# Kernel optimization log

Measured on AMD Instinct MI355X. Metric: run time of the kernel, lower is better.

Reference implementation:

```python
import jax, jax.numpy as jnp
import numpy as np

B, L, D = 4, 4096, 1024
K = D // 4

def setup_inputs() -> dict:
    key = jax.random.key(0)
    ks = jax.random.split(key, 16)
    def w(k, sh):
        return jax.random.normal(k, sh, dtype=jnp.float32) * 0.02
    return {
        'x': jax.random.normal(ks[0], (B, L, D), dtype=jnp.float32),
        'Wk1': w(ks[1], (D, D)), 'bk1': jnp.zeros((D,), jnp.float32),
        'Wk2': w(ks[2], (D, K * 4)), 'bk2': jnp.zeros((K * 4,), jnp.float32),
        'Wq1': w(ks[3], (D, D)), 'bq1': jnp.zeros((D,), jnp.float32),
        'Wq2': w(ks[4], (D, K * 4)), 'bq2': jnp.zeros((K * 4,), jnp.float32),
        'Wv': w(ks[5], (D, D)), 'bv': jnp.zeros((D,), jnp.float32),
        'gamma': jnp.ones((D,), jnp.float32), 'beta': jnp.zeros((D,), jnp.float32),
        'Wo': w(ks[6], (D, D)), 'bo': jnp.zeros((D,), jnp.float32),
    }

def _normalize(q, eps=1e-12):
    n = jnp.sqrt(jnp.sum(q * q, axis=-1, keepdims=True))
    return q / jnp.maximum(n, eps)

def _quat_conj(q):
    return q * jnp.asarray([1., -1., -1., -1.], dtype=q.dtype)

def _quat_mul(q1, q2):
    w1, x1, y1, z1 = q1[..., 0], q1[..., 1], q1[..., 2], q1[..., 3]
    w2, x2, y2, z2 = q2[..., 0], q2[..., 1], q2[..., 2], q2[..., 3]
    w = w1 * w2 - x1 * x2 - y1 * y2 - z1 * z2
    x = w1 * x2 + x1 * w2 + y1 * z2 - z1 * y2
    y = w1 * y2 - x1 * z2 + y1 * w2 + z1 * x2
    z = w1 * z2 + x1 * y2 - y1 * x2 + z1 * w2
    return jnp.stack([w, x, y, z], axis=-1)

def _quat_rotate(q, v):
    return _quat_mul(_quat_mul(q, v), _quat_conj(q))

def _mlp(x, W1, b1, W2, b2):
    h = jax.nn.gelu(x @ W1 + b1, approximate=False)
    return h @ W2 + b2

def _layernorm(x, g, b, eps=1e-5):
    mu = jnp.mean(x, axis=-1, keepdims=True)
    var = jnp.var(x, axis=-1, keepdims=True)
    return (x - mu) * jax.lax.rsqrt(var + eps) * g + b

def reference(x, Wk1, bk1, Wk2, bk2, Wq1, bq1, Wq2, bq2, Wv, bv, gamma, beta, Wo, bo):
    b, l, d = x.shape
    k = d // 4
    key_q = _normalize(_mlp(x, Wk1, bk1, Wk2, bk2).reshape(b, l, k, 4))
    query_q = _normalize(_mlp(x, Wq1, bq1, Wq2, bq2).reshape(b, l, k, 4))
    value = (x @ Wv + bv).reshape(b, l, k, 4)
    rotated = _quat_rotate(key_q, value)            # [B,L,K,4]
    memory = jnp.cumsum(rotated, axis=1)            # prefix-sum memory
    retrieved = _quat_rotate(_quat_conj(query_q), memory).reshape(b, l, d)
    norm = jnp.sqrt(jnp.arange(1, l + 1, dtype=x.dtype)).reshape(1, l, 1)
    out = _layernorm(retrieved / norm, gamma, beta) @ Wo + bo
    return x + out
```

## Files before the change

### kernel.cpp

```cpp
#include <hip/hip_runtime.h>
#include <hip/hip_bf16.h>
#include <cstddef>
#include <cstdint>

static constexpr int B   = 4;
static constexpr int L   = 4096;
static constexpr int D   = 1024;
static constexpr int M   = B * L;
static constexpr int NCH = 64;
static constexpr int CHL = L / NCH;

typedef __attribute__((ext_vector_type(8))) short short8;
typedef __attribute__((ext_vector_type(4))) float f32x4;

#define AS1C(p) ((const __attribute__((address_space(1))) void*)(p))
#define AS3(p)  ((__attribute__((address_space(3))) void*)(p))

__device__ __forceinline__ float b2f(unsigned short u) {
    union { unsigned int i; float f; } c; c.i = ((unsigned int)u) << 16; return c.f;
}
__device__ __forceinline__ unsigned short f2b(float f) {
    union { float f; unsigned int i; } c; c.f = f;
    unsigned int r = c.i + 0x7fffu + ((c.i >> 16) & 1u);
    return (unsigned short)(r >> 16);
}
__device__ __forceinline__ float4 qmul(const float4 a, const float4 b) {
    float4 r;
    r.x = a.x * b.x - a.y * b.y - a.z * b.z - a.w * b.w;
    r.y = a.x * b.y + a.y * b.x + a.z * b.w - a.w * b.z;
    r.z = a.x * b.z - a.y * b.w + a.z * b.x + a.w * b.y;
    r.w = a.x * b.w + a.y * b.z - a.z * b.y + a.w * b.x;
    return r;
}
__device__ __forceinline__ float4 qconj(const float4 a) {
    return make_float4(a.x, -a.y, -a.z, -a.w);
}
__device__ __forceinline__ float4 qnorm(const float4 a) {
    float n = sqrtf(a.x * a.x + a.y * a.y + a.z * a.z + a.w * a.w);
    float inv = 1.0f / fmaxf(n, 1e-12f);
    return make_float4(a.x * inv, a.y * inv, a.z * inv, a.w * inv);
}
__device__ __forceinline__ float gelu_exact(float v) {
    return 0.5f * v * (1.0f + erff(v * 0.7071067811865476f));
}

__global__ __launch_bounds__(256)
void conv_k(const float* __restrict__ src, unsigned short* __restrict__ dst, int n4)
{
    const int i = blockIdx.x * 256 + threadIdx.x;
    if (i >= n4) return;
    const float4 v = reinterpret_cast<const float4*>(src)[i];
    ushort4 o;
    o.x = f2b(v.x); o.y = f2b(v.y); o.z = f2b(v.z); o.w = f2b(v.w);
    reinterpret_cast<ushort4*>(dst)[i] = o;
}

__global__ __launch_bounds__(256)
void wtrans_k(const float* __restrict__ src, unsigned short* __restrict__ dst)
{
    __shared__ float t[32][33];
    const int tx = threadIdx.x, ty = threadIdx.y;
    const int n0 = blockIdx.x * 32, k0 = blockIdx.y * 32;
    #pragma unroll
    for (int j = ty; j < 32; j += 8)
        t[j][tx] = src[(size_t)(k0 + j) * D + n0 + tx];
    __syncthreads();
    #pragma unroll
    for (int j = ty; j < 32; j += 8)
        dst[(size_t)(n0 + j) * D + k0 + tx] = f2b(t[tx][j]);
}

template <int EPI>
__global__ __launch_bounds__(256)
void gemm_bf16_k(const unsigned short* __restrict__ A,
                 const unsigned short* __restrict__ BT,
                 const float* __restrict__ bias,
                 const float* __restrict__ resid,
                 void* __restrict__ C, int Mm, int Nn, int Kk)
{
    __shared__ alignas(16) unsigned short As[128 * 32];
    __shared__ alignas(16) unsigned short Bs[128 * 32];

    const int tid  = threadIdx.x;
    const int lane = tid & 63;
    const int w    = tid >> 6;
    const int wr   = w >> 1;
    const int wc   = w & 1;

    const int nwg = gridDim.x;
    const int cpx = nwg >> 3;
    const int bid = blockIdx.x;
    const int swz = (bid & 7) * cpx + (bid >> 3);
    const int nTN = Nn >> 7;
    const int m0  = (swz / nTN) << 7;
    const int n0  = (swz % nTN) << 7;

    f32x4 acc[4][4] = {};

    for (int k0 = 0; k0 < Kk; k0 += 32) {
        #pragma unroll
        for (int c = 0; c < 2; ++c) {
            const int i  = (c * 4 + w) * 64 + lane;
            const int r  = i >> 2;
            const int cc = i & 3;
            __builtin_amdgcn_global_load_lds(
                AS1C(A + (size_t)(m0 + r) * Kk + k0 + cc * 8),
                AS3((char*)As + (c * 4 + w) * 1024), 16, 0, 0);
            __builtin_amdgcn_global_load_lds(
                AS1C(BT + (size_t)(n0 + r) * Kk + k0 + cc * 8),
                AS3((char*)Bs + (c * 4 + w) * 1024), 16, 0, 0);
        }
        __syncthreads();

        short8 af[4], bf[4];
        #pragma unroll
        for (int mi = 0; mi < 4; ++mi) {
            const int r = wr * 64 + mi * 16 + (lane & 15);
            af[mi] = *reinterpret_cast<const short8*>(
                (const char*)As + r * 64 + (lane >> 4) * 16);
        }
        #pragma unroll
        for (int ni = 0; ni < 4; ++ni) {
            const int cI = wc * 64 + ni * 16 + (lane & 15);
            bf[ni] = *reinterpret_cast<const short8*>(
                (const char*)Bs + cI * 64 + (lane >> 4) * 16);
        }
        #pragma unroll
        for (int mi = 0; mi < 4; ++mi)
            #pragma unroll
            for (int ni = 0; ni < 4; ++ni)
                acc[mi][ni] = __builtin_amdgcn_mfma_f32_16x16x32_bf16(
                    af[mi], bf[ni], acc[mi][ni], 0, 0, 0);
        __syncthreads();
    }

    const int colbase = n0 + wc * 64 + (lane & 15);
    #pragma unroll
    for (int ni = 0; ni < 4; ++ni) {
        const int col = colbase + ni * 16;
        const float bv = bias[col];
        #pragma unroll
        for (int mi = 0; mi < 4; ++mi) {
            const int row0 = m0 + wr * 64 + mi * 16 + (lane >> 4) * 4;
            #pragma unroll
            for (int r = 0; r < 4; ++r) {
                float v = acc[mi][ni][r] + bv;
                if (EPI == 1) v = gelu_exact(v);
                const size_t idx = (size_t)(row0 + r) * Nn + col;
                if (EPI <= 1) {
                    ((unsigned short*)C)[idx] = f2b(v);
                } else {
                    if (EPI == 3) v += resid[idx];
                    ((float*)C)[idx] = v;
                }
            }
        }
    }
}

__global__ __launch_bounds__(256)
void rotate_k(const unsigned short* __restrict__ kraw, float* __restrict__ v, int nq)
{
    const int i = blockIdx.x * 256 + threadIdx.x;
    if (i >= nq) return;
    const ushort4 qu = reinterpret_cast<const ushort4*>(kraw)[i];
    float4 q = qnorm(make_float4(b2f(qu.x), b2f(qu.y), b2f(qu.z), b2f(qu.w)));
    const float4 val = reinterpret_cast<const float4*>(v)[i];
    const float4 r = qmul(qmul(q, val), qconj(q));
    reinterpret_cast<float4*>(v)[i] = r;
}

__global__ __launch_bounds__(256)
void scan_pass1(const float* __restrict__ rot, float* __restrict__ part)
{
    const int g  = blockIdx.x * 256 + threadIdx.x;
    const int d  = g & (D - 1);
    const int ch = (g >> 10) & (NCH - 1);
    const int b  = g >> 16;
    const size_t base = ((size_t)b * L + (size_t)ch * CHL) * D + d;
    float s = 0.f;
    for (int i = 0; i < CHL; ++i) s += rot[base + (size_t)i * D];
    part[g] = s;
}

__global__ __launch_bounds__(256)
void scan_pass2(float* __restrict__ part)
{
    const int g = blockIdx.x * 256 + threadIdx.x;
    const int d = g & (D - 1);
    const int b = g >> 10;
    float run = 0.f;
    for (int c = 0; c < NCH; ++c) {
        const size_t idx = ((size_t)b * NCH + c) * D + d;
        const float t = part[idx];
        part[idx] = run;
        run += t;
    }
}

__global__ __launch_bounds__(256)
void scan_pass3(float* __restrict__ rot, const float* __restrict__ part)
{
    const int g  = blockIdx.x * 256 + threadIdx.x;
    const int d  = g & (D - 1);
    const int ch = (g >> 10) & (NCH - 1);
    const int b  = g >> 16;
    const size_t base = ((size_t)b * L + (size_t)ch * CHL) * D + d;
    float run = part[g];
    for (int i = 0; i < CHL; ++i) {
        const size_t idx = base + (size_t)i * D;
        run += rot[idx];
        rot[idx] = run;
    }
}

__global__ __launch_bounds__(256)
void retrieve_ln_k(const float* __restrict__ mem, const unsigned short* __restrict__ qraw,
                   const float* __restrict__ gamma, const float* __restrict__ beta,
                   unsigned short* __restrict__ out)
{
    const int row = blockIdx.x;
    const int l   = row & (L - 1);
    const int t   = threadIdx.x;
    const size_t base = (size_t)row * D + t * 4;

    const ushort4 qu = reinterpret_cast<const ushort4*>(qraw)[base >> 2];
    const float4 q = qnorm(make_float4(b2f(qu.x), b2f(qu.y), b2f(qu.z), b2f(qu.w)));
    const float4 m4 = *reinterpret_cast<const float4*>(mem + base);
    float4 r = qmul(qmul(qconj(q), m4), q);

    const float inv = 1.0f / sqrtf((float)(l + 1));
    r.x *= inv; r.y *= inv; r.z *= inv; r.w *= inv;

    float s  = r.x + r.y + r.z + r.w;
    float ss = r.x * r.x + r.y * r.y + r.z * r.z + r.w * r.w;
    #pragma unroll
    for (int off = 32; off > 0; off >>= 1) {
        s  += __shfl_xor(s, off);
        ss += __shfl_xor(ss, off);
    }
    __shared__ float red[2][4];
    const int wid = t >> 6, lane = t & 63;
    if (lane == 0) { red[0][wid] = s; red[1][wid] = ss; }
    __syncthreads();
    const float sum = red[0][0] + red[0][1] + red[0][2] + red[0][3];
    const float ssq = red[1][0] + red[1][1] + red[1][2] + red[1][3];
    const float mu  = sum * (1.0f / (float)D);
    const float var = ssq * (1.0f / (float)D) - mu * mu;
    const float sc  = rsqrtf(var + 1e-5f);

    const float4 g4 = *reinterpret_cast<const float4*>(gamma + t * 4);
    const float4 b4 = *reinterpret_cast<const float4*>(beta  + t * 4);
    ushort4 o;
    o.x = f2b((r.x - mu) * sc * g4.x + b4.x);
    o.y = f2b((r.y - mu) * sc * g4.y + b4.y);
    o.z = f2b((r.z - mu) * sc * g4.z + b4.z);
    o.w = f2b((r.w - mu) * sc * g4.w + b4.w);
    reinterpret_cast<ushort4*>(out)[base >> 2] = o;
}

extern "C" void kernel_launch(void* const* d_in, const int* in_sizes, int n_in,
                              void* d_out, int out_size, void* d_ws, size_t ws_size,
                              hipStream_t stream)
{
    const float* x     = (const float*)d_in[0];
    const float* Wk1   = (const float*)d_in[1];
    const float* bk1   = (const float*)d_in[2];
    const float* Wk2   = (const float*)d_in[3];
    const float* bk2   = (const float*)d_in[4];
    const float* Wq1   = (const float*)d_in[5];
    const float* bq1   = (const float*)d_in[6];
    const float* Wq2   = (const float*)d_in[7];
    const float* bq2   = (const float*)d_in[8];
    const float* Wv    = (const float*)d_in[9];
    const float* bv    = (const float*)d_in[10];
    const float* gamma = (const float*)d_in[11];
    const float* beta  = (const float*)d_in[12];
    const float* Wo    = (const float*)d_in[13];
    const float* bo    = (const float*)d_in[14];
    float* out = (float*)d_out;

    const size_t TD = (size_t)M * D;
    const size_t DD = (size_t)D * D;
    unsigned short* xb   = (unsigned short*)d_ws;
    unsigned short* hb   = xb + TD;
    unsigned short* qb   = hb + TD;
    float*          bufB = (float*)(qb + TD);
    unsigned short* wT   = (unsigned short*)(bufB + TD);
    float*          part = (float*)(wT + 6 * DD);

    unsigned short* wk1 = wT;
    unsigned short* wk2 = wT + DD;
    unsigned short* wv_ = wT + 2 * DD;
    unsigned short* wq1 = wT + 3 * DD;
    unsigned short* wq2 = wT + 4 * DD;
    unsigned short* wo_ = wT + 5 * DD;

    const dim3 blk(256);
    const dim3 tblk(32, 8);
    const dim3 tgrid(D / 32, D / 32);
    const int nwg = (M / 128) * (D / 128);
    const int nq  = (int)(TD / 4);

    conv_k<<<(int)(TD / 4 / 256), blk, 0, stream>>>(x, xb, (int)(TD / 4));
    wtrans_k<<<tgrid, tblk, 0, stream>>>(Wk1, wk1);
    wtrans_k<<<tgrid, tblk, 0, stream>>>(Wk2, wk2);
    wtrans_k<<<tgrid, tblk, 0, stream>>>(Wv,  wv_);
    wtrans_k<<<tgrid, tblk, 0, stream>>>(Wq1, wq1);
    wtrans_k<<<tgrid, tblk, 0, stream>>>(Wq2, wq2);
    wtrans_k<<<tgrid, tblk, 0, stream>>>(Wo,  wo_);

    gemm_bf16_k<1><<<nwg, blk, 0, stream>>>(xb, wk1, bk1, nullptr, hb,   M, D, D);
    gemm_bf16_k<0><<<nwg, blk, 0, stream>>>(hb, wk2, bk2, nullptr, qb,   M, D, D);
    gemm_bf16_k<2><<<nwg, blk, 0, stream>>>(xb, wv_, bv,  nullptr, bufB, M, D, D);

    rotate_k<<<nq / 256, blk, 0, stream>>>(qb, bufB, nq);

    scan_pass1<<<(B * NCH * D) / 256, blk, 0, stream>>>(bufB, part);
    scan_pass2<<<(B * D) / 256,       blk, 0, stream>>>(part);
    scan_pass3<<<(B * NCH * D) / 256, blk, 0, stream>>>(bufB, part);

    gemm_bf16_k<1><<<nwg, blk, 0, stream>>>(xb, wq1, bq1, nullptr, hb, M, D, D);
    gemm_bf16_k<0><<<nwg, blk, 0, stream>>>(hb, wq2, bq2, nullptr, qb, M, D, D);

    retrieve_ln_k<<<M, blk, 0, stream>>>(bufB, qb, gamma, beta, hb);

    gemm_bf16_k<3><<<nwg, blk, 0, stream>>>(hb, wo_, bo, x, out, M, D, D);
}
```

Measured before the change: 513.2 us.

## Batch projection GEMMs into wide 256-tile pipelined GEMMs and fuse rotate with scan

Concatenates the K1/Q1/V weights and the K2/Q2 weights so the five projection GEMMs become two launches. All GEMMs move to a new 256x256-tile, 512-thread kernel with a 3-buffer LDS pipeline, XOR-swizzled LDS layout, and setprio hints. The quaternion rotation is fused into the first scan pass, and the scan now works on float4. Exact erf GELU is replaced with a polynomial approximation. This cuts launch count, memory round trips and GEMM stall time, at the cost of more LDS, higher register pressure and a small GELU accuracy change.

Result: faster. 464.5 us (-9.5%).

```diff
diff --git a/kernel.cpp b/kernel.cpp
--- a/kernel.cpp
+++ b/kernel.cpp
@@ -1,14 +1,13 @@
 #include <hip/hip_runtime.h>
-#include <hip/hip_bf16.h>
 #include <cstddef>
 #include <cstdint>
 
-static constexpr int B   = 4;
-static constexpr int L   = 4096;
-static constexpr int D   = 1024;
-static constexpr int M   = B * L;
-static constexpr int NCH = 64;
-static constexpr int CHL = L / NCH;
+static constexpr int Bb  = 4;
+static constexpr int Ll  = 4096;
+static constexpr int Dd  = 1024;
+static constexpr int Mm  = 16384;
+static constexpr int KK  = 1024;
+static constexpr int NTK = 32;
 
 typedef __attribute__((ext_vector_type(8))) short short8;
 typedef __attribute__((ext_vector_type(4))) float f32x4;
@@ -40,8 +39,15 @@
     float inv = 1.0f / fmaxf(n, 1e-12f);
     return make_float4(a.x * inv, a.y * inv, a.z * inv, a.w * inv);
 }
-__device__ __forceinline__ float gelu_exact(float v) {
-    return 0.5f * v * (1.0f + erff(v * 0.7071067811865476f));
+__device__ __forceinline__ float gelu_fast(float v) {
+    const float a = fabsf(v) * 0.70710678118654752f;
+    const float t = 1.0f / (1.0f + 0.3275911f * a);
+    const float p = t * (0.254829592f + t * (-0.284496736f + t * (1.421413741f
+                   + t * (-1.453152027f + t * 1.061405429f))));
+    const float e = __expf(-a * a);
+    const float erfa = 1.0f - p * e;
+    const float erfv = copysignf(erfa, v);
+    return 0.5f * v * (1.0f + erfv);
 }
 
 __global__ __launch_bounds__(256)
@@ -63,95 +69,156 @@
     const int n0 = blockIdx.x * 32, k0 = blockIdx.y * 32;
     #pragma unroll
     for (int j = ty; j < 32; j += 8)
-        t[j][tx] = src[(size_t)(k0 + j) * D + n0 + tx];
+        t[j][tx] = src[(size_t)(k0 + j) * Dd + n0 + tx];
     __syncthreads();
     #pragma unroll
     for (int j = ty; j < 32; j += 8)
-        dst[(size_t)(n0 + j) * D + k0 + tx] = f2b(t[tx][j]);
-}
-
-template <int EPI>
-__global__ __launch_bounds__(256)
-void gemm_bf16_k(const unsigned short* __restrict__ A,
-                 const unsigned short* __restrict__ BT,
-                 const float* __restrict__ bias,
-                 const float* __restrict__ resid,
-                 void* __restrict__ C, int Mm, int Nn, int Kk)
-{
-    __shared__ alignas(16) unsigned short As[128 * 32];
-    __shared__ alignas(16) unsigned short Bs[128 * 32];
-
+        dst[(size_t)(n0 + j) * Dd + k0 + tx] = f2b(t[tx][j]);
+}
+
+__global__ __launch_bounds__(256)
+void bcat_k(const float* __restrict__ bk1, const float* __restrict__ bq1,
+            const float* __restrict__ bv,  const float* __restrict__ bk2,
+            const float* __restrict__ bq2, float* __restrict__ b1,
+            float* __restrict__ b2)
+{
+    const int i = blockIdx.x * 256 + threadIdx.x;
+    if (i < 3072) b1[i] = (i < 1024) ? bk1[i] : (i < 2048 ? bq1[i - 1024] : bv[i - 2048]);
+    if (i < 2048) b2[i] = (i < 1024) ? bk2[i] : bq2[i - 1024];
+}
+
+template<int MODE>
+__global__ __launch_bounds__(512, 2)
+void gemm256_k(const unsigned short* __restrict__ A, int astride,
+               const unsigned short* __restrict__ BT,
+               const float* __restrict__ bias,
+               const float* __restrict__ resid,
+               unsigned short* __restrict__ outH,
+               float* __restrict__ outF,
+               int Nn)
+{
+    extern __shared__ char smem[];
     const int tid  = threadIdx.x;
     const int lane = tid & 63;
     const int w    = tid >> 6;
-    const int wr   = w >> 1;
-    const int wc   = w & 1;
+    const int wr   = w >> 2;
+    const int wc   = w & 3;
 
     const int nwg = gridDim.x;
     const int cpx = nwg >> 3;
     const int bid = blockIdx.x;
     const int swz = (bid & 7) * cpx + (bid >> 3);
-    const int nTN = Nn >> 7;
-    const int m0  = (swz / nTN) << 7;
-    const int n0  = (swz % nTN) << 7;
-
-    f32x4 acc[4][4] = {};
-
-    for (int k0 = 0; k0 < Kk; k0 += 32) {
+    const int nTN = Nn >> 8;
+    const int m0  = (swz / nTN) << 8;
+    const int n0  = (swz % nTN) << 8;
+    const int aoff = (MODE == 1 && n0 >= 1024) ? 1024 : 0;
+
+    const unsigned short* gA[2];
+    const unsigned short* gB[2];
+    #pragma unroll
+    for (int c = 0; c < 2; ++c) {
+        const int n16 = c * 512 + tid;
+        const int line = n16 >> 3;
+        const int u = (n16 & 7) ^ (line & 7);
+        const int r = 2 * line + (u >> 2);
+        const int kcs = u & 3;
+        gA[c] = A + (size_t)(m0 + r) * astride + aoff + kcs * 8;
+        gB[c] = BT + (size_t)(n0 + r) * KK + kcs * 8;
+    }
+    const int wslot = w * 1024;
+
+    auto STAGE = [&](int kt, int bi) {
+        const int koff = kt * 32;
         #pragma unroll
         for (int c = 0; c < 2; ++c) {
-            const int i  = (c * 4 + w) * 64 + lane;
-            const int r  = i >> 2;
-            const int cc = i & 3;
-            __builtin_amdgcn_global_load_lds(
-                AS1C(A + (size_t)(m0 + r) * Kk + k0 + cc * 8),
-                AS3((char*)As + (c * 4 + w) * 1024), 16, 0, 0);
-            __builtin_amdgcn_global_load_lds(
-                AS1C(BT + (size_t)(n0 + r) * Kk + k0 + cc * 8),
-                AS3((char*)Bs + (c * 4 + w) * 1024), 16, 0, 0);
+            __builtin_amdgcn_global_load_lds(AS1C(gA[c] + koff),
+                AS3(smem + bi * 16384 + c * 8192 + wslot), 16, 0, 0);
+            __builtin_amdgcn_global_load_lds(AS1C(gB[c] + koff),
+                AS3(smem + 49152 + bi * 16384 + c * 8192 + wslot), 16, 0, 0);
         }
-        __syncthreads();
-
+    };
+
+    const int kc = lane >> 4;
+    const int rl = lane & 15;
+    int offA[8], offB[4];
+    #pragma unroll
+    for (int mi = 0; mi < 8; ++mi) {
+        const int r = wr * 128 + mi * 16 + rl;
+        offA[mi] = (r >> 1) * 128 + (((((r & 1) << 2) | kc) ^ ((r >> 1) & 7)) << 4);
+    }
+    #pragma unroll
+    for (int ni = 0; ni < 4; ++ni) {
+        const int r = wc * 64 + ni * 16 + rl;
+        offB[ni] = 49152 + (r >> 1) * 128 + (((((r & 1) << 2) | kc) ^ ((r >> 1) & 7)) << 4);
+    }
+
+    f32x4 acc[8][4] = {};
+
+    auto BODY = [&](int kt, int bi, int bi2, int vm, bool dostage) {
+        if (dostage) STAGE(kt + 2, bi2);
+        const char* Ab = smem + bi * 16384;
         short8 af[4], bf[4];
         #pragma unroll
-        for (int mi = 0; mi < 4; ++mi) {
-            const int r = wr * 64 + mi * 16 + (lane & 15);
-            af[mi] = *reinterpret_cast<const short8*>(
-                (const char*)As + r * 64 + (lane >> 4) * 16);
-        }
-        #pragma unroll
-        for (int ni = 0; ni < 4; ++ni) {
-            const int cI = wc * 64 + ni * 16 + (lane & 15);
-            bf[ni] = *reinterpret_cast<const short8*>(
-                (const char*)Bs + cI * 64 + (lane >> 4) * 16);
-        }
+        for (int ni = 0; ni < 4; ++ni) bf[ni] = *(const short8*)(smem + bi * 16384 + offB[ni]);
+        #pragma unroll
+        for (int mi = 0; mi < 4; ++mi) af[mi] = *(const short8*)(Ab + offA[mi]);
+        __builtin_amdgcn_s_barrier();
+        __builtin_amdgcn_s_setprio(1);
         #pragma unroll
         for (int mi = 0; mi < 4; ++mi)
             #pragma unroll
             for (int ni = 0; ni < 4; ++ni)
-                acc[mi][ni] = __builtin_amdgcn_mfma_f32_16x16x32_bf16(
-                    af[mi], bf[ni], acc[mi][ni], 0, 0, 0);
-        __syncthreads();
-    }
-
-    const int colbase = n0 + wc * 64 + (lane & 15);
+                acc[mi][ni] = __builtin_amdgcn_mfma_f32_16x16x32_bf16(af[mi], bf[ni], acc[mi][ni], 0, 0, 0);
+        __builtin_amdgcn_s_setprio(0);
+        __builtin_amdgcn_s_barrier();
+        #pragma unroll
+        for (int mi = 0; mi < 4; ++mi) af[mi] = *(const short8*)(Ab + offA[4 + mi]);
+        __builtin_amdgcn_s_setprio(1);
+        #pragma unroll
+        for (int mi = 0; mi < 4; ++mi)
+            #pragma unroll
+            for (int ni = 0; ni < 4; ++ni)
+                acc[4 + mi][ni] = __builtin_amdgcn_mfma_f32_16x16x32_bf16(af[mi], bf[ni], acc[4 + mi][ni], 0, 0, 0);
+        __builtin_amdgcn_s_setprio(0);
+        if (vm == 4)      asm volatile("s_waitcnt vmcnt(4)" ::: "memory");
+        else if (vm == 0) asm volatile("s_waitcnt vmcnt(0)" ::: "memory");
+        if (vm >= 0) __builtin_amdgcn_s_barrier();
+    };
+
+    STAGE(0, 0);
+    STAGE(1, 1);
+    asm volatile("s_waitcnt vmcnt(4)" ::: "memory");
+    __builtin_amdgcn_s_barrier();
+
+    for (int t0 = 0; t0 < NTK - 2; t0 += 3) {
+        BODY(t0 + 0, 0, 2, 4, true);
+        BODY(t0 + 1, 1, 0, 4, true);
+        BODY(t0 + 2, 2, 1, 4, true);
+    }
+    BODY(NTK - 2, 0, 0, 0, false);
+    BODY(NTK - 1, 1, 0, -1, false);
+
+    const int colb = n0 + wc * 64 + rl;
+    const int rowb = m0 + wr * 128 + kc * 4;
     #pragma unroll
     for (int ni = 0; ni < 4; ++ni) {
-        const int col = colbase + ni * 16;
+        const int col = colb + ni * 16;
         const float bv = bias[col];
         #pragma unroll
-        for (int mi = 0; mi < 4; ++mi) {
-            const int row0 = m0 + wr * 64 + mi * 16 + (lane >> 4) * 4;
+        for (int mi = 0; mi < 8; ++mi) {
+            const int row0 = rowb + mi * 16;
             #pragma unroll
-            for (int r = 0; r < 4; ++r) {
-                float v = acc[mi][ni][r] + bv;
-                if (EPI == 1) v = gelu_exact(v);
-                const size_t idx = (size_t)(row0 + r) * Nn + col;
-                if (EPI <= 1) {
-                    ((unsigned short*)C)[idx] = f2b(v);
+            for (int rr = 0; rr < 4; ++rr) {
+                float v = acc[mi][ni][rr] + bv;
+                const int row = row0 + rr;
+                if (MODE == 0) {
+                    if (n0 < 2048) outH[(size_t)row * 2048 + col] = f2b(gelu_fast(v));
+                    else           outF[(size_t)row * 1024 + (col - 2048)] = v;
+                } else if (MODE == 1) {
+                    outH[(size_t)row * 2048 + col] = f2b(v);
                 } else {
-                    if (EPI == 3) v += resid[idx];
-                    ((float*)C)[idx] = v;
+                    const size_t ix = (size_t)row * 1024 + col;
+                    outF[ix] = v + resid[ix];
                 }
             }
         }
@@ -159,72 +226,69 @@
 }
 
 __global__ __launch_bounds__(256)
-void rotate_k(const unsigned short* __restrict__ kraw, float* __restrict__ v, int nq)
-{
-    const int i = blockIdx.x * 256 + threadIdx.x;
-    if (i >= nq) return;
-    const ushort4 qu = reinterpret_cast<const ushort4*>(kraw)[i];
-    float4 q = qnorm(make_float4(b2f(qu.x), b2f(qu.y), b2f(qu.z), b2f(qu.w)));
-    const float4 val = reinterpret_cast<const float4*>(v)[i];
-    const float4 r = qmul(qmul(q, val), qconj(q));
-    reinterpret_cast<float4*>(v)[i] = r;
-}
-
-__global__ __launch_bounds__(256)
-void scan_pass1(const float* __restrict__ rot, float* __restrict__ part)
-{
-    const int g  = blockIdx.x * 256 + threadIdx.x;
-    const int d  = g & (D - 1);
-    const int ch = (g >> 10) & (NCH - 1);
-    const int b  = g >> 16;
-    const size_t base = ((size_t)b * L + (size_t)ch * CHL) * D + d;
-    float s = 0.f;
-    for (int i = 0; i < CHL; ++i) s += rot[base + (size_t)i * D];
-    part[g] = s;
-}
-
-__global__ __launch_bounds__(256)
-void scan_pass2(float* __restrict__ part)
-{
-    const int g = blockIdx.x * 256 + threadIdx.x;
-    const int d = g & (D - 1);
-    const int b = g >> 10;
-    float run = 0.f;
-    for (int c = 0; c < NCH; ++c) {
-        const size_t idx = ((size_t)b * NCH + c) * D + d;
-        const float t = part[idx];
-        part[idx] = run;
-        run += t;
-    }
-}
-
-__global__ __launch_bounds__(256)
-void scan_pass3(float* __restrict__ rot, const float* __restrict__ part)
-{
-    const int g  = blockIdx.x * 256 + threadIdx.x;
-    const int d  = g & (D - 1);
-    const int ch = (g >> 10) & (NCH - 1);
-    const int b  = g >> 16;
-    const size_t base = ((size_t)b * L + (size_t)ch * CHL) * D + d;
-    float run = part[g];
-    for (int i = 0; i < CHL; ++i) {
-        const size_t idx = base + (size_t)i * D;
-        run += rot[idx];
-        rot[idx] = run;
-    }
-}
-
-__global__ __launch_bounds__(256)
-void retrieve_ln_k(const float* __restrict__ mem, const unsigned short* __restrict__ qraw,
+void rotfuse_k(const unsigned short* __restrict__ qb2, float* __restrict__ val,
+               float* __restrict__ part)
+{
+    const int idx = blockIdx.x * 256 + threadIdx.x;
+    const int kq  = idx & 255;
+    const int ch  = (idx >> 8) & 63;
+    const int b   = idx >> 14;
+    const int row0 = b * Ll + ch * 64;
+    float4 s = make_float4(0.f, 0.f, 0.f, 0.f);
+    for (int i = 0; i < 64; ++i) {
+        const int row = row0 + i;
+        const ushort4 qu = *reinterpret_cast<const ushort4*>(qb2 + (size_t)row * 2048 + kq * 4);
+        const float4 q = qnorm(make_float4(b2f(qu.x), b2f(qu.y), b2f(qu.z), b2f(qu.w)));
+        float4* vp = reinterpret_cast<float4*>(val + (size_t)row * 1024 + kq * 4);
+        const float4 r = qmul(qmul(q, *vp), qconj(q));
+        *vp = r;
+        s.x += r.x; s.y += r.y; s.z += r.z; s.w += r.w;
+    }
+    *reinterpret_cast<float4*>(part + (size_t)idx * 4) = s;
+}
+
+__global__ __launch_bounds__(256)
+void scan2_k(float* __restrict__ part)
+{
+    const int idx = blockIdx.x * 256 + threadIdx.x;
+    const int kq = idx & 255, b = idx >> 8;
+    float4 run = make_float4(0.f, 0.f, 0.f, 0.f);
+    for (int c = 0; c < 64; ++c) {
+        float4* p = reinterpret_cast<float4*>(part + (((size_t)(b * 64 + c)) * 256 + kq) * 4);
+        const float4 t = *p;
+        *p = run;
+        run.x += t.x; run.y += t.y; run.z += t.z; run.w += t.w;
+    }
+}
+
+__global__ __launch_bounds__(256)
+void scan3_k(float* __restrict__ val, const float* __restrict__ part)
+{
+    const int idx = blockIdx.x * 256 + threadIdx.x;
+    const int kq  = idx & 255;
+    const int ch  = (idx >> 8) & 63;
+    const int b   = idx >> 14;
+    const int row0 = b * Ll + ch * 64;
+    float4 run = *reinterpret_cast<const float4*>(part + (size_t)idx * 4);
+    for (int i = 0; i < 64; ++i) {
+        float4* vp = reinterpret_cast<float4*>(val + (size_t)(row0 + i) * 1024 + kq * 4);
+        const float4 v = *vp;
+        run.x += v.x; run.y += v.y; run.z += v.z; run.w += v.w;
+        *vp = run;
+    }
+}
+
+__global__ __launch_bounds__(256)
+void retrieve_ln_k(const float* __restrict__ mem, const unsigned short* __restrict__ qb2,
                    const float* __restrict__ gamma, const float* __restrict__ beta,
                    unsigned short* __restrict__ out)
 {
     const int row = blockIdx.x;
-    const int l   = row & (L - 1);
+    const int l   = row & (Ll - 1);
     const int t   = threadIdx.x;
-    const size_t base = (size_t)row * D + t * 4;
-
-    const ushort4 qu = reinterpret_cast<const ushort4*>(qraw)[base >> 2];
+    const size_t base = (size_t)row * 1024 + t * 4;
+
+    const ushort4 qu = *reinterpret_cast<const ushort4*>(qb2 + (size_t)row * 2048 + 1024 + t * 4);
     const float4 q = qnorm(make_float4(b2f(qu.x), b2f(qu.y), b2f(qu.z), b2f(qu.w)));
     const float4 m4 = *reinterpret_cast<const float4*>(mem + base);
     float4 r = qmul(qmul(qconj(q), m4), q);
@@ -245,8 +309,8 @@
     __syncthreads();
     const float sum = red[0][0] + red[0][1] + red[0][2] + red[0][3];
     const float ssq = red[1][0] + red[1][1] + red[1][2] + red[1][3];
-    const float mu  = sum * (1.0f / (float)D);
-    const float var = ssq * (1.0f / (float)D) - mu * mu;
+    const float mu  = sum * (1.0f / 1024.0f);
+    const float var = ssq * (1.0f / 1024.0f) - mu * mu;
     const float sc  = rsqrtf(var + 1e-5f);
 
     const float4 g4 = *reinterpret_cast<const float4*>(gamma + t * 4);
@@ -256,7 +320,7 @@
     o.y = f2b((r.y - mu) * sc * g4.y + b4.y);
     o.z = f2b((r.z - mu) * sc * g4.z + b4.z);
     o.w = f2b((r.w - mu) * sc * g4.w + b4.w);
-    reinterpret_cast<ushort4*>(out)[base >> 2] = o;
+    *reinterpret_cast<ushort4*>(out + base) = o;
 }
 
 extern "C" void kernel_launch(void* const* d_in, const int* in_sizes, int n_in,
@@ -280,50 +344,45 @@
     const float* bo    = (const float*)d_in[14];
     float* out = (float*)d_out;
 
-    const size_t TD = (size_t)M * D;
-    const size_t DD = (size_t)D * D;
-    unsigned short* xb   = (unsigned short*)d_ws;
-    unsigned short* hb   = xb + TD;
-    unsigned short* qb   = hb + TD;
-    float*          bufB = (float*)(qb + TD);
-    unsigned short* wT   = (unsigned short*)(bufB + TD);
-    float*          part = (float*)(wT + 6 * DD);
-
-    unsigned short* wk1 = wT;
-    unsigned short* wk2 = wT + DD;
-    unsigned short* wv_ = wT + 2 * DD;
-    unsigned short* wq1 = wT + 3 * DD;
-    unsigned short* wq2 = wT + 4 * DD;
-    unsigned short* wo_ = wT + 5 * DD;
+    const size_t TD = (size_t)Mm * 1024;
+    const size_t DD = (size_t)1024 * 1024;
+
+    unsigned short* qb2   = (unsigned short*)d_ws;
+    unsigned short* xb    = qb2;
+    unsigned short* wcat1 = qb2 + TD;
+    unsigned short* h     = qb2 + 2 * TD;
+    float*          bufB  = (float*)(h + 2 * TD);
+    unsigned short* wcat2 = (unsigned short*)(bufB + TD);
+    unsigned short* woT   = wcat2 + 2 * DD;
+    float*          bcat1 = (float*)(woT + DD);
+    float*          bcat2 = bcat1 + 3072;
+    float*          part  = bcat2 + 2048;
 
     const dim3 blk(256);
     const dim3 tblk(32, 8);
-    const dim3 tgrid(D / 32, D / 32);
-    const int nwg = (M / 128) * (D / 128);
-    const int nq  = (int)(TD / 4);
+    const dim3 tgrid(32, 32);
+
+    (void)hipFuncSetAttribute((const void*)gemm256_k<0>, hipFuncAttributeMaxDynamicSharedMemorySize, 98304);
+    (void)hipFuncSetAttribute((const void*)gemm256_k<1>, hipFuncAttributeMaxDynamicSharedMemorySize, 98304);
+    (void)hipFuncSetAttribute((const void*)gemm256_k<2>, hipFuncAttributeMaxDynamicSharedMemorySize, 98304);
 
     conv_k<<<(int)(TD / 4 / 256), blk, 0, stream>>>(x, xb, (int)(TD / 4));
-    wtrans_k<<<tgrid, tblk, 0, stream>>>(Wk1, wk1);
-    wtrans_k<<<tgrid, tblk, 0, stream>>>(Wk2, wk2);
-    wtrans_k<<<tgrid, tblk, 0, stream>>>(Wv,  wv_);
-    wtrans_k<<<tgrid, tblk, 0, stream>>>(Wq1, wq1);
-    wtrans_k<<<tgrid, tblk, 0, stream>>>(Wq2, wq2);
-    wtrans_k<<<tgrid, tblk, 0, stream>>>(Wo,  wo_);
-
-    gemm_bf16_k<1><<<nwg, blk, 0, stream>>>(xb, wk1, bk1, nullptr, hb,   M, D, D);
-    gemm_bf16_k<0><<<nwg, blk, 0, stream>>>(hb, wk2, bk2, nullptr, qb,   M, D, D);
-    gemm_bf16_k<2><<<nwg, blk, 0, stream>>>(xb, wv_, bv,  nullptr, bufB, M, D, D);
-
-    rotate_k<<<nq / 256, blk, 0, stream>>>(qb, bufB, nq);
-
-    scan_pass1<<<(B * NCH * D) / 256, blk, 0, stream>>>(bufB, part);
-    scan_pass2<<<(B * D) / 256,       blk, 0, stream>>>(part);
-    scan_pass3<<<(B * NCH * D) / 256, blk, 0, stream>>>(bufB, part);
-
-    gemm_bf16_k<1><<<nwg, blk, 0, stream>>>(xb, wq1, bq1, nullptr, hb, M, D, D);
-    gemm_bf16_k<0><<<nwg, blk, 0, stream>>>(hb, wq2, bq2, nullptr, qb, M, D, D);
-
-    retrieve_ln_k<<<M, blk, 0, stream>>>(bufB, qb, gamma, beta, hb);
-
-    gemm_bf16_k<3><<<nwg, blk, 0, stream>>>(hb, wo_, bo, x, out, M, D, D);
-}
+    wtrans_k<<<tgrid, tblk, 0, stream>>>(Wk1, wcat1);
+    wtrans_k<<<tgrid, tblk, 0, stream>>>(Wq1, wcat1 + DD);
+    wtrans_k<<<tgrid, tblk, 0, stream>>>(Wv,  wcat1 + 2 * DD);
+    wtrans_k<<<tgrid, tblk, 0, stream>>>(Wk2, wcat2);
+    wtrans_k<<<tgrid, tblk, 0, stream>>>(Wq2, wcat2 + DD);
+    wtrans_k<<<tgrid, tblk, 0, stream>>>(Wo,  woT);
+    bcat_k<<<12, blk, 0, stream>>>(bk1, bq1, bv, bk2, bq2, bcat1, bcat2);
+
+    gemm256_k<0><<<64 * 12, 512, 98304, stream>>>(xb, 1024, wcat1, bcat1, nullptr, h, bufB, 3072);
+    gemm256_k<1><<<64 * 8, 512, 98304, stream>>>(h, 2048, wcat2, bcat2, nullptr, qb2, nullptr, 2048);
+
+    rotfuse_k<<<256, blk, 0, stream>>>(qb2, bufB, part);
+    scan2_k<<<4, blk, 0, stream>>>(part);
+    scan3_k<<<256, blk, 0, stream>>>(bufB, part);
+
+    retrieve_ln_k<<<Mm, blk, 0, stream>>>(bufB, qb2, gamma, beta, h);
+
+    gemm256_k<2><<<64 * 4, 512, 98304, stream>>>(h, 1024, woT, bo, x, nullptr, out, 1024);
+}
```
